# Optimization experiments

Hardware: AMD Instinct MI355X
Metric: run time of the kernel (lower is better)

Reference implementation:

```python
import jax, jax.numpy as jnp
import numpy as np

D = 1024

def setup_inputs() -> dict:
    key = jax.random.key(0)
    ks = jax.random.split(key, 7)
    s = 1.0 / np.sqrt(D)
    x = jax.random.normal(ks[0], (8, 2048, D), dtype=jnp.float32)
    Wq = jax.random.uniform(ks[1], (D, D), jnp.float32, -s, s)
    bq = jax.random.uniform(ks[2], (D,), jnp.float32, -s, s)
    Wk = jax.random.uniform(ks[3], (D, D), jnp.float32, -s, s)
    bk = jax.random.uniform(ks[4], (D,), jnp.float32, -s, s)
    Wv = jax.random.uniform(ks[5], (D, D), jnp.float32, -s, s)
    bv = jax.random.uniform(ks[6], (D,), jnp.float32, -s, s)
    return {"x": x, "Wq": Wq, "bq": bq, "Wk": Wk, "bk": bk, "Wv": Wv, "bv": bv}

def reference(x, Wq, bq, Wk, bk, Wv, bv):
    # x: [B, N, D]; Linear weights stored [D, D] used as x @ W + b (W = torch weight.T)
    q = x @ Wq + bq
    k = x @ Wk + bk
    v = x @ Wv + bv
    scores = jnp.einsum('bnd,bmd->bnm', q, k) / jnp.sqrt(jnp.float32(x.shape[-1]))
    attn = jax.nn.softmax(scores, axis=2)
    return jnp.einsum('bnm,bmd->bnd', attn, v)
```

## Files before the change

kernel.cpp:

```cpp
#include <hip/hip_runtime.h>
#include <hip/hip_bf16.h>

typedef unsigned short u16;
typedef short bf16x8 __attribute__((ext_vector_type(8)));
typedef float f32x16 __attribute__((ext_vector_type(16)));
typedef unsigned short u16x8 __attribute__((ext_vector_type(8)));
typedef unsigned short u16x4 __attribute__((ext_vector_type(4)));

__device__ __forceinline__ u16 f2bf(float f) {
    unsigned u = __float_as_uint(f);
    return (u16)((u + 0x7FFFu + ((u >> 16) & 1u)) >> 16);
}
__device__ __forceinline__ float bf2f(u16 h) {
    return __uint_as_float(((unsigned)h) << 16);
}

__global__ __launch_bounds__(256) void cast_f32_bf16(const float4* __restrict__ src,
                                                     ushort4* __restrict__ dst, int n4) {
    int i = blockIdx.x * 256 + threadIdx.x;
    if (i < n4) {
        float4 v = src[i];
        ushort4 o;
        o.x = f2bf(v.x); o.y = f2bf(v.y); o.z = f2bf(v.z); o.w = f2bf(v.w);
        dst[i] = o;
    }
}

__global__ __launch_bounds__(256) void transpose_cast3(const float* __restrict__ W0,
                                                       const float* __restrict__ W1,
                                                       const float* __restrict__ W2,
                                                       u16* __restrict__ WT) {
    __shared__ float t[32][33];
    const float* W = (blockIdx.z == 0) ? W0 : (blockIdx.z == 1) ? W1 : W2;
    u16* Wt = WT + (long)blockIdx.z * 1048576;
    int bx = blockIdx.x * 32;
    int by = blockIdx.y * 32;
    int tx = threadIdx.x, ty = threadIdx.y;
    for (int r = ty; r < 32; r += 8)
        t[r][tx] = W[(by + r) * 1024 + bx + tx];
    __syncthreads();
    for (int r = ty; r < 32; r += 8)
        Wt[(long)(bx + r) * 1024 + by + tx] = f2bf(t[tx][r]);
}

template <int MODE>
__global__ __launch_bounds__(256)
void gemm_bt(const u16* __restrict__ A, int lda, long sA,
             const u16* __restrict__ Bt, int ldb, long sB,
             const float* __restrict__ bq_, const float* __restrict__ bk_,
             const float* __restrict__ bv_,
             void* __restrict__ Cout, void* __restrict__ Cout2,
             int ldc, long sC, int Kdim, float scale)
{
    __shared__ __align__(16) u16 As[128 * 64];
    __shared__ __align__(16) u16 Bs[128 * 64];
    const int tid  = threadIdx.x;
    const int wave = tid >> 6;
    const int lane = tid & 63;
    const int m32  = lane & 31;
    const int hi   = lane >> 5;

    const int gx = gridDim.x, gy = gridDim.y;
    int flat = (blockIdx.z * gy + blockIdx.y) * gx + blockIdx.x;
    int total = gx * gy * gridDim.z;
    int tile = (flat & 7) * (total >> 3) + (flat >> 3);
    const int bx = tile % gx;
    const int by = (tile / gx) % gy;
    const int bz = tile / (gx * gy);

    const u16* Ab = A + (long)bz * sA;
    const u16* Bb = Bt + (long)bz * sB;
    const int row0 = by * 128;
    const int col0 = bx * 128;
    const int wr = (wave & 1) * 64;
    const int wc = (wave >> 1) * 64;

    f32x16 acc[2][2] = {};

    int arow[2], brow[2], asw[2], bsw[2];
#pragma unroll
    for (int t = 0; t < 2; ++t) {
        arow[t] = wr + t * 32 + m32;
        brow[t] = wc + t * 32 + m32;
        asw[t] = arow[t] & 7;
        bsw[t] = brow[t] & 7;
    }

    for (int k0 = 0; k0 < Kdim; k0 += 64) {
#pragma unroll
        for (int it = 0; it < 4; ++it) {
            int c = it * 256 + tid;
            int r = c >> 3;
            int kc = (c & 7) ^ (r & 7);
            const u16* ga = Ab + (long)(row0 + r) * lda + (k0 + kc * 8);
            __builtin_amdgcn_global_load_lds(
                (const __attribute__((address_space(1))) void*)ga,
                (__attribute__((address_space(3))) void*)(&As[c * 8]), 16, 0, 0);
            const u16* gb = Bb + (long)(col0 + r) * ldb + (k0 + kc * 8);
            __builtin_amdgcn_global_load_lds(
                (const __attribute__((address_space(1))) void*)gb,
                (__attribute__((address_space(3))) void*)(&Bs[c * 8]), 16, 0, 0);
        }
        __syncthreads();
#pragma unroll
        for (int kh = 0; kh < 4; ++kh) {
            bf16x8 af[2], bfr[2];
#pragma unroll
            for (int t = 0; t < 2; ++t) {
                int qa = (kh * 2 + hi) ^ asw[t];
                int qb = (kh * 2 + hi) ^ bsw[t];
                af[t]  = *(const bf16x8*)&As[arow[t] * 64 + qa * 8];
                bfr[t] = *(const bf16x8*)&Bs[brow[t] * 64 + qb * 8];
            }
#pragma unroll
            for (int i = 0; i < 2; ++i)
#pragma unroll
                for (int j = 0; j < 2; ++j)
                    acc[i][j] = __builtin_amdgcn_mfma_f32_32x32x16_bf16(
                        af[i], bfr[j], acc[i][j], 0, 0, 0);
        }
        __syncthreads();
    }

    if (MODE == 0) {
        if (col0 < 2048) {
            const float* bp = (col0 < 1024) ? bq_ : bk_;
#pragma unroll
            for (int i = 0; i < 2; ++i) {
#pragma unroll
                for (int j = 0; j < 2; ++j) {
                    int col = col0 + wc + j * 32 + m32;
                    float badd = bp[col & 1023];
#pragma unroll
                    for (int g = 0; g < 4; ++g) {
                        int rbase = row0 + wr + i * 32 + 4 * hi + 8 * g;
#pragma unroll
                        for (int rr = 0; rr < 4; ++rr)
                            ((u16*)Cout)[(long)(rbase + rr) * 2048 + col] =
                                f2bf(acc[i][j][g * 4 + rr] + badd);
                    }
                }
            }
        } else {
#pragma unroll
            for (int i = 0; i < 2; ++i) {
#pragma unroll
                for (int j = 0; j < 2; ++j) {
                    int d = col0 + wc + j * 32 + m32 - 2048;
                    float badd = bv_[d];
#pragma unroll
                    for (int g = 0; g < 4; ++g) {
                        int rbase = row0 + wr + i * 32 + 4 * hi + 8 * g;
                        int b = rbase >> 11, m = rbase & 2047;
                        u16x4 pk;
#pragma unroll
                        for (int rr = 0; rr < 4; ++rr)
                            pk[rr] = f2bf(acc[i][j][g * 4 + rr] + badd);
                        *(u16x4*)((u16*)Cout2 + ((long)b << 21) + ((long)d << 11) + m) = pk;
                    }
                }
            }
        }
    } else {
#pragma unroll
        for (int i = 0; i < 2; ++i) {
#pragma unroll
            for (int j = 0; j < 2; ++j) {
                int col = col0 + wc + j * 32 + m32;
#pragma unroll
                for (int g = 0; g < 4; ++g) {
                    int rbase = row0 + wr + i * 32 + 4 * hi + 8 * g;
#pragma unroll
                    for (int rr = 0; rr < 4; ++rr) {
                        int row = rbase + rr;
                        float v = acc[i][j][g * 4 + rr];
                        if (MODE == 2) {
                            ((u16*)Cout)[(long)bz * sC + (long)row * ldc + col] = f2bf(v * scale);
                        } else {
                            ((float*)Cout)[(long)bz * sC + (long)row * ldc + col] = v;
                        }
                    }
                }
            }
        }
    }
}

__global__ __launch_bounds__(256) void softmax_rows(u16* __restrict__ S) {
    __shared__ float red[4];
    const long row = blockIdx.x;
    u16* p = S + row * 2048;
    const int tid = threadIdx.x;
    const int lane = tid & 63, wv = tid >> 6;

    u16x8 raw = *(const u16x8*)(p + tid * 8);
    float v[8];
#pragma unroll
    for (int i = 0; i < 8; ++i) v[i] = bf2f(raw[i]);

    float m = -1e30f;
#pragma unroll
    for (int i = 0; i < 8; ++i) m = fmaxf(m, v[i]);
    for (int off = 32; off > 0; off >>= 1) m = fmaxf(m, __shfl_down(m, off));
    if (lane == 0) red[wv] = m;
    __syncthreads();
    m = fmaxf(fmaxf(red[0], red[1]), fmaxf(red[2], red[3]));

    float s = 0.0f;
#pragma unroll
    for (int i = 0; i < 8; ++i) { v[i] = __expf(v[i] - m); s += v[i]; }
    for (int off = 32; off > 0; off >>= 1) s += __shfl_down(s, off);
    __syncthreads();
    if (lane == 0) red[wv] = s;
    __syncthreads();
    s = red[0] + red[1] + red[2] + red[3];
    float inv = 1.0f / s;

    u16x8 o;
#pragma unroll
    for (int i = 0; i < 8; ++i) o[i] = f2bf(v[i] * inv);
    *(u16x8*)(p + tid * 8) = o;
}

extern "C" void kernel_launch(void* const* d_in, const int* in_sizes, int n_in,
                              void* d_out, int out_size, void* d_ws, size_t ws_size,
                              hipStream_t stream) {
    const float* x  = (const float*)d_in[0];
    const float* Wq = (const float*)d_in[1];
    const float* bq = (const float*)d_in[2];
    const float* Wk = (const float*)d_in[3];
    const float* bk = (const float*)d_in[4];
    const float* Wv = (const float*)d_in[5];
    const float* bv = (const float*)d_in[6];
    float* out = (float*)d_out;

    char* ws = (char*)d_ws;
    u16* xb = (u16*)(ws);
    u16* WT = (u16*)(ws + 33554432);
    u16* QK = (u16*)(ws + 39845888);
    u16* Vt = (u16*)(ws + 106954752);
    u16* S  = (u16*)(ws + 140509184);

    cast_f32_bf16<<<16384, 256, 0, stream>>>((const float4*)x, (ushort4*)xb, 4194304);
    dim3 tg(32, 32, 3), tb(32, 8);
    transpose_cast3<<<tg, tb, 0, stream>>>(Wq, Wk, Wv, WT);

    dim3 gp(24, 128, 1);
    gemm_bt<0><<<gp, 256, 0, stream>>>(xb, 1024, 0, WT, 1024, 0,
                                       bq, bk, bv, QK, Vt, 0, 0, 1024, 1.0f);

    dim3 gs(16, 16, 8);
    gemm_bt<2><<<gs, 256, 0, stream>>>(QK, 2048, 2048L * 2048, QK + 1024, 2048, 2048L * 2048,
                                       nullptr, nullptr, nullptr, S, nullptr,
                                       2048, 2048L * 2048, 1024, 0.03125f);

    softmax_rows<<<16384, 256, 0, stream>>>(S);

    dim3 gv(8, 16, 8);
    gemm_bt<3><<<gv, 256, 0, stream>>>(S, 2048, 2048L * 2048, Vt, 2048, 1024L * 2048,
                                       nullptr, nullptr, nullptr, out, nullptr,
                                       1024, 2048L * 1024, 2048, 1.0f);
}
```

Measured before the change: 424.0 us.

## Restructure GEMM to 256x256 tiles with 4-stage async LDS pipeline

Rewrites the shared GEMM kernel used for the QKV projection, QK^T and PV products. It now uses 512-thread blocks computing 256x256 output tiles with BK=32 and 16x16x32 bf16 MFMAs. A 4-deep ring of LDS buffers is filled via global_load_lds with explicit vmcnt waits, so loads overlap compute instead of sync-load-sync per k-step. The aim is more data reuse per block and better latency hiding. In exchange it uses 128KB of LDS and about 128 accumulator VGPRs per thread, which limits occupancy to one block per CU. Each block also covers more of the output, so fewer blocks are launched.

Result: faster. 394.4 us (-7.0%).

```diff
diff --git a/kernel.cpp b/kernel.cpp
--- a/kernel.cpp
+++ b/kernel.cpp
@@ -3,7 +3,7 @@
 
 typedef unsigned short u16;
 typedef short bf16x8 __attribute__((ext_vector_type(8)));
-typedef float f32x16 __attribute__((ext_vector_type(16)));
+typedef float f32x4 __attribute__((ext_vector_type(4)));
 typedef unsigned short u16x8 __attribute__((ext_vector_type(8)));
 typedef unsigned short u16x4 __attribute__((ext_vector_type(4)));
 
@@ -43,8 +43,20 @@
         Wt[(long)(bx + r) * 1024 + by + tx] = f2bf(t[tx][r]);
 }
 
+#define GLL16(g, l)                                                     \
+    __builtin_amdgcn_global_load_lds(                                   \
+        (const __attribute__((address_space(1))) void*)(g),             \
+        (__attribute__((address_space(3))) void*)(l), 16, 0, 0)
+
+#define PIPE_WAIT_BAR(vmstr)                                            \
+    do {                                                                \
+        asm volatile("s_waitcnt " vmstr " lgkmcnt(0)" ::: "memory");    \
+        __builtin_amdgcn_s_barrier();                                   \
+        asm volatile("" ::: "memory");                                  \
+    } while (0)
+
 template <int MODE>
-__global__ __launch_bounds__(256)
+__global__ __launch_bounds__(512, 2)
 void gemm_bt(const u16* __restrict__ A, int lda, long sA,
              const u16* __restrict__ Bt, int ldb, long sB,
              const float* __restrict__ bq_, const float* __restrict__ bk_,
@@ -52,13 +64,13 @@
              void* __restrict__ Cout, void* __restrict__ Cout2,
              int ldc, long sC, int Kdim, float scale)
 {
-    __shared__ __align__(16) u16 As[128 * 64];
-    __shared__ __align__(16) u16 Bs[128 * 64];
+    __shared__ __align__(16) u16 lds[4 * 16384];
+
     const int tid  = threadIdx.x;
     const int wave = tid >> 6;
     const int lane = tid & 63;
-    const int m32  = lane & 31;
-    const int hi   = lane >> 5;
+    const int lrow = lane & 15;
+    const int kc   = lane >> 4;
 
     const int gx = gridDim.x, gy = gridDim.y;
     int flat = (blockIdx.z * gy + blockIdx.y) * gx + blockIdx.x;
@@ -70,116 +82,121 @@
 
     const u16* Ab = A + (long)bz * sA;
     const u16* Bb = Bt + (long)bz * sB;
-    const int row0 = by * 128;
-    const int col0 = bx * 128;
-    const int wr = (wave & 1) * 64;
+    const int row0 = by * 256;
+    const int col0 = bx * 256;
+    const int wr = (wave & 1) * 128;
     const int wc = (wave >> 1) * 64;
 
-    f32x16 acc[2][2] = {};
-
-    int arow[2], brow[2], asw[2], bsw[2];
-#pragma unroll
-    for (int t = 0; t < 2; ++t) {
-        arow[t] = wr + t * 32 + m32;
-        brow[t] = wc + t * 32 + m32;
-        asw[t] = arow[t] & 7;
-        bsw[t] = brow[t] & 7;
-    }
-
-    for (int k0 = 0; k0 < Kdim; k0 += 64) {
-#pragma unroll
-        for (int it = 0; it < 4; ++it) {
-            int c = it * 256 + tid;
-            int r = c >> 3;
-            int kc = (c & 7) ^ (r & 7);
-            const u16* ga = Ab + (long)(row0 + r) * lda + (k0 + kc * 8);
-            __builtin_amdgcn_global_load_lds(
-                (const __attribute__((address_space(1))) void*)ga,
-                (__attribute__((address_space(3))) void*)(&As[c * 8]), 16, 0, 0);
-            const u16* gb = Bb + (long)(col0 + r) * ldb + (k0 + kc * 8);
-            __builtin_amdgcn_global_load_lds(
-                (const __attribute__((address_space(1))) void*)gb,
-                (__attribute__((address_space(3))) void*)(&Bs[c * 8]), 16, 0, 0);
-        }
-        __syncthreads();
-#pragma unroll
-        for (int kh = 0; kh < 4; ++kh) {
-            bf16x8 af[2], bfr[2];
-#pragma unroll
-            for (int t = 0; t < 2; ++t) {
-                int qa = (kh * 2 + hi) ^ asw[t];
-                int qb = (kh * 2 + hi) ^ bsw[t];
-                af[t]  = *(const bf16x8*)&As[arow[t] * 64 + qa * 8];
-                bfr[t] = *(const bf16x8*)&Bs[brow[t] * 64 + qb * 8];
-            }
-#pragma unroll
-            for (int i = 0; i < 2; ++i)
-#pragma unroll
-                for (int j = 0; j < 2; ++j)
-                    acc[i][j] = __builtin_amdgcn_mfma_f32_32x32x16_bf16(
-                        af[i], bfr[j], acc[i][j], 0, 0, 0);
-        }
-        __syncthreads();
-    }
-
+    const int rS = tid >> 2;
+    const int cS = (tid & 3) ^ ((tid >> 3) & 3);
+    const u16* pa0 = Ab + (long)(row0 + rS) * lda + cS * 8;
+    const u16* pa1 = pa0 + (long)128 * lda;
+    const u16* pb0 = Bb + (long)(col0 + rS) * ldb + cS * 8;
+    const u16* pb1 = pb0 + (long)128 * ldb;
+    const int dA0 = tid * 8, dA1 = 4096 + tid * 8;
+    const int dB0 = 8192 + tid * 8, dB1 = 12288 + tid * 8;
+
+    int offA[8], offB[4];
+#pragma unroll
+    for (int mf = 0; mf < 8; ++mf) {
+        int r = wr + mf * 16 + lrow;
+        offA[mf] = r * 32 + (kc ^ ((r >> 1) & 3)) * 8;
+    }
+#pragma unroll
+    for (int nf = 0; nf < 4; ++nf) {
+        int r = wc + nf * 16 + lrow;
+        offB[nf] = 8192 + r * 32 + (kc ^ ((r >> 1) & 3)) * 8;
+    }
+
+    f32x4 acc[8][4] = {};
+
+    auto stage = [&](int t) {
+        u16* lb = &lds[(t & 3) * 16384];
+        int ko = t * 32;
+        GLL16(pa0 + ko, lb + dA0);
+        GLL16(pa1 + ko, lb + dA1);
+        GLL16(pb0 + ko, lb + dB0);
+        GLL16(pb1 + ko, lb + dB1);
+    };
+
+    auto compute = [&](int t) {
+        const u16* lb = &lds[(t & 3) * 16384];
+        bf16x8 af[8], bfr[4];
+#pragma unroll
+        for (int nf = 0; nf < 4; ++nf) bfr[nf] = *(const bf16x8*)&lb[offB[nf]];
+#pragma unroll
+        for (int mf = 0; mf < 8; ++mf) af[mf] = *(const bf16x8*)&lb[offA[mf]];
+        __builtin_amdgcn_s_setprio(1);
+#pragma unroll
+        for (int mf = 0; mf < 8; ++mf)
+#pragma unroll
+            for (int nf = 0; nf < 4; ++nf)
+                acc[mf][nf] = __builtin_amdgcn_mfma_f32_16x16x32_bf16(
+                    af[mf], bfr[nf], acc[mf][nf], 0, 0, 0);
+        __builtin_amdgcn_s_setprio(0);
+    };
+
+    const int NT = Kdim >> 5;
+    stage(0); stage(1); stage(2);
+    for (int t = 0; t < NT - 3; ++t) {
+        PIPE_WAIT_BAR("vmcnt(8)");
+        stage(t + 3);
+        compute(t);
+    }
+    PIPE_WAIT_BAR("vmcnt(8)");
+    compute(NT - 3);
+    PIPE_WAIT_BAR("vmcnt(4)");
+    compute(NT - 2);
+    PIPE_WAIT_BAR("vmcnt(0)");
+    compute(NT - 1);
+
+    const int lq = kc;
     if (MODE == 0) {
         if (col0 < 2048) {
             const float* bp = (col0 < 1024) ? bq_ : bk_;
 #pragma unroll
-            for (int i = 0; i < 2; ++i) {
-#pragma unroll
-                for (int j = 0; j < 2; ++j) {
-                    int col = col0 + wc + j * 32 + m32;
+            for (int mf = 0; mf < 8; ++mf) {
+#pragma unroll
+                for (int nf = 0; nf < 4; ++nf) {
+                    int col = col0 + wc + nf * 16 + lrow;
                     float badd = bp[col & 1023];
-#pragma unroll
-                    for (int g = 0; g < 4; ++g) {
-                        int rbase = row0 + wr + i * 32 + 4 * hi + 8 * g;
-#pragma unroll
-                        for (int rr = 0; rr < 4; ++rr)
-                            ((u16*)Cout)[(long)(rbase + rr) * 2048 + col] =
-                                f2bf(acc[i][j][g * 4 + rr] + badd);
-                    }
+                    int rbase = row0 + wr + mf * 16 + lq * 4;
+#pragma unroll
+                    for (int g = 0; g < 4; ++g)
+                        ((u16*)Cout)[(long)(rbase + g) * 2048 + col] =
+                            f2bf(acc[mf][nf][g] + badd);
                 }
             }
         } else {
 #pragma unroll
-            for (int i = 0; i < 2; ++i) {
-#pragma unroll
-                for (int j = 0; j < 2; ++j) {
-                    int d = col0 + wc + j * 32 + m32 - 2048;
+            for (int mf = 0; mf < 8; ++mf) {
+#pragma unroll
+                for (int nf = 0; nf < 4; ++nf) {
+                    int d = col0 + wc + nf * 16 + lrow - 2048;
                     float badd = bv_[d];
-#pragma unroll
-                    for (int g = 0; g < 4; ++g) {
-                        int rbase = row0 + wr + i * 32 + 4 * hi + 8 * g;
-                        int b = rbase >> 11, m = rbase & 2047;
-                        u16x4 pk;
-#pragma unroll
-                        for (int rr = 0; rr < 4; ++rr)
-                            pk[rr] = f2bf(acc[i][j][g * 4 + rr] + badd);
-                        *(u16x4*)((u16*)Cout2 + ((long)b << 21) + ((long)d << 11) + m) = pk;
-                    }
+                    int rbase = row0 + wr + mf * 16 + lq * 4;
+                    int b = rbase >> 11, m = rbase & 2047;
+                    u16x4 pk;
+#pragma unroll
+                    for (int g = 0; g < 4; ++g) pk[g] = f2bf(acc[mf][nf][g] + badd);
+                    *(u16x4*)((u16*)Cout2 + ((long)b << 21) + ((long)d << 11) + m) = pk;
                 }
             }
         }
     } else {
 #pragma unroll
-        for (int i = 0; i < 2; ++i) {
-#pragma unroll
-            for (int j = 0; j < 2; ++j) {
-                int col = col0 + wc + j * 32 + m32;
+        for (int mf = 0; mf < 8; ++mf) {
+#pragma unroll
+            for (int nf = 0; nf < 4; ++nf) {
+                int col = col0 + wc + nf * 16 + lrow;
+                int rbase = row0 + wr + mf * 16 + lq * 4;
 #pragma unroll
                 for (int g = 0; g < 4; ++g) {
-                    int rbase = row0 + wr + i * 32 + 4 * hi + 8 * g;
-#pragma unroll
-                    for (int rr = 0; rr < 4; ++rr) {
-                        int row = rbase + rr;
-                        float v = acc[i][j][g * 4 + rr];
-                        if (MODE == 2) {
-                            ((u16*)Cout)[(long)bz * sC + (long)row * ldc + col] = f2bf(v * scale);
-                        } else {
-                            ((float*)Cout)[(long)bz * sC + (long)row * ldc + col] = v;
-                        }
-                    }
+                    long idx = (long)bz * sC + (long)(rbase + g) * ldc + col;
+                    if (MODE == 2)
+                        ((u16*)Cout)[idx] = f2bf(acc[mf][nf][g] * scale);
+                    else
+                        ((float*)Cout)[idx] = acc[mf][nf][g];
                 }
             }
         }
@@ -245,19 +262,19 @@
     dim3 tg(32, 32, 3), tb(32, 8);
     transpose_cast3<<<tg, tb, 0, stream>>>(Wq, Wk, Wv, WT);
 
-    dim3 gp(24, 128, 1);
-    gemm_bt<0><<<gp, 256, 0, stream>>>(xb, 1024, 0, WT, 1024, 0,
+    dim3 gp(12, 64, 1);
+    gemm_bt<0><<<gp, 512, 0, stream>>>(xb, 1024, 0, WT, 1024, 0,
                                        bq, bk, bv, QK, Vt, 0, 0, 1024, 1.0f);
 
-    dim3 gs(16, 16, 8);
-    gemm_bt<2><<<gs, 256, 0, stream>>>(QK, 2048, 2048L * 2048, QK + 1024, 2048, 2048L * 2048,
+    dim3 gs(8, 8, 8);
+    gemm_bt<2><<<gs, 512, 0, stream>>>(QK, 2048, 2048L * 2048, QK + 1024, 2048, 2048L * 2048,
                                        nullptr, nullptr, nullptr, S, nullptr,
                                        2048, 2048L * 2048, 1024, 0.03125f);
 
     softmax_rows<<<16384, 256, 0, stream>>>(S);
 
-    dim3 gv(8, 16, 8);
-    gemm_bt<3><<<gv, 256, 0, stream>>>(S, 2048, 2048L * 2048, Vt, 2048, 1024L * 2048,
+    dim3 gv(4, 8, 8);
+    gemm_bt<3><<<gv, 512, 0, stream>>>(S, 2048, 2048L * 2048, Vt, 2048, 1024L * 2048,
                                        nullptr, nullptr, nullptr, out, nullptr,
                                        1024, 2048L * 1024, 2048, 1.0f);
 }
```

## Enlarge GEMM tiles to 256x256 with double-buffered LDS pipeline

Applied to the files above, without the earlier changes.

Switches the bf16 GEMM kernel to 512-thread blocks computing 256x256 tiles, with two LDS buffers. The next K-tile's global-to-LDS loads are issued in quarter-steps, gated by vmcnt waits and barriers, and MFMA priority is raised while computing. The aim is to overlap memory latency with matrix math and raise data reuse per loaded byte. In exchange, each block now uses 128 KB of LDS, and the PV GEMM launches fewer, larger blocks, which reduces parallelism.

Result: slower. 642.0 us (+51.4%).

```diff
diff --git a/kernel.cpp b/kernel.cpp
--- a/kernel.cpp
+++ b/kernel.cpp
@@ -43,8 +43,19 @@
         Wt[(long)(bx + r) * 1024 + by + tx] = f2bf(t[tx][r]);
 }
 
+#define GLL16(g, l)                                                     \
+    __builtin_amdgcn_global_load_lds(                                   \
+        (const __attribute__((address_space(1))) void*)(g),             \
+        (__attribute__((address_space(3))) void*)(l), 16, 0, 0)
+
+#define VMB(n)                                                          \
+    do {                                                                \
+        asm volatile("s_waitcnt vmcnt(" #n ")" ::: "memory");           \
+        __builtin_amdgcn_s_barrier();                                   \
+    } while (0)
+
 template <int MODE>
-__global__ __launch_bounds__(256)
+__global__ __launch_bounds__(512, 2)
 void gemm_bt(const u16* __restrict__ A, int lda, long sA,
              const u16* __restrict__ Bt, int ldb, long sB,
              const float* __restrict__ bq_, const float* __restrict__ bk_,
@@ -52,13 +63,13 @@
              void* __restrict__ Cout, void* __restrict__ Cout2,
              int ldc, long sC, int Kdim, float scale)
 {
-    __shared__ __align__(16) u16 As[128 * 64];
-    __shared__ __align__(16) u16 Bs[128 * 64];
+    __shared__ __align__(16) u16 lds[2 * 32768];
+
     const int tid  = threadIdx.x;
     const int wave = tid >> 6;
     const int lane = tid & 63;
     const int m32  = lane & 31;
-    const int hi   = lane >> 5;
+    const int hi5  = lane >> 5;
 
     const int gx = gridDim.x, gy = gridDim.y;
     int flat = (blockIdx.z * gy + blockIdx.y) * gx + blockIdx.x;
@@ -70,70 +81,77 @@
 
     const u16* Ab = A + (long)bz * sA;
     const u16* Bb = Bt + (long)bz * sB;
-    const int row0 = by * 128;
-    const int col0 = bx * 128;
-    const int wr = (wave & 1) * 64;
+    const int row0 = by * 256;
+    const int col0 = bx * 256;
+    const int wr = (wave & 1) * 128;
     const int wc = (wave >> 1) * 64;
 
-    f32x16 acc[2][2] = {};
-
-    int arow[2], brow[2], asw[2], bsw[2];
-#pragma unroll
-    for (int t = 0; t < 2; ++t) {
-        arow[t] = wr + t * 32 + m32;
-        brow[t] = wc + t * 32 + m32;
-        asw[t] = arow[t] & 7;
-        bsw[t] = brow[t] & 7;
-    }
-
-    for (int k0 = 0; k0 < Kdim; k0 += 64) {
-#pragma unroll
-        for (int it = 0; it < 4; ++it) {
-            int c = it * 256 + tid;
-            int r = c >> 3;
-            int kc = (c & 7) ^ (r & 7);
-            const u16* ga = Ab + (long)(row0 + r) * lda + (k0 + kc * 8);
-            __builtin_amdgcn_global_load_lds(
-                (const __attribute__((address_space(1))) void*)ga,
-                (__attribute__((address_space(3))) void*)(&As[c * 8]), 16, 0, 0);
-            const u16* gb = Bb + (long)(col0 + r) * ldb + (k0 + kc * 8);
-            __builtin_amdgcn_global_load_lds(
-                (const __attribute__((address_space(1))) void*)gb,
-                (__attribute__((address_space(3))) void*)(&Bs[c * 8]), 16, 0, 0);
+    const int r255 = tid & 255;
+    const int hp   = tid >> 8;
+    const u16* paA = Ab + (long)(row0 + r255) * lda + hp * 8;
+    const u16* pbB = Bb + (long)(col0 + r255) * ldb + hp * 8;
+    const int dst8 = tid * 8;
+
+    const int aoff = hi5 * 2048 + (wr + m32) * 8;
+    const int boff = 16384 + hi5 * 2048 + (wc + m32) * 8;
+
+    f32x16 acc[4][2] = {};
+
+#define STAGE_G(t, g)                                                       \
+    do {                                                                    \
+        u16* lb_ = &lds[((t) & 1) * 32768];                                 \
+        const long ko_ = (long)(t) * 64 + (g) * 16;                         \
+        GLL16(paA + ko_, lb_ + (g) * 4096 + dst8);                          \
+        GLL16(pbB + ko_, lb_ + 16384 + (g) * 4096 + dst8);                  \
+    } while (0)
+
+#define READ_MMA(lb_, p)                                                    \
+    do {                                                                    \
+        bf16x8 af[4], bfr[2];                                               \
+        _Pragma("unroll") for (int i = 0; i < 4; ++i)                       \
+            af[i] = *(const bf16x8*)&(lb_)[(p) * 4096 + aoff + i * 256];    \
+        _Pragma("unroll") for (int j = 0; j < 2; ++j)                       \
+            bfr[j] = *(const bf16x8*)&(lb_)[(p) * 4096 + boff + j * 256];   \
+        __builtin_amdgcn_s_setprio(1);                                      \
+        _Pragma("unroll") for (int i = 0; i < 4; ++i)                       \
+        _Pragma("unroll") for (int j = 0; j < 2; ++j)                       \
+            acc[i][j] = __builtin_amdgcn_mfma_f32_32x32x16_bf16(            \
+                af[i], bfr[j], acc[i][j], 0, 0, 0);                         \
+        __builtin_amdgcn_s_setprio(0);                                      \
+    } while (0)
+
+    const int NT = Kdim >> 6;
+    STAGE_G(0, 0); STAGE_G(0, 1); STAGE_G(0, 2); STAGE_G(0, 3);
+
+    for (int t = 0; t < NT - 1; ++t) {
+        const u16* lb = &lds[(t & 1) * 32768];
+#pragma unroll
+        for (int p = 0; p < 4; ++p) {
+            VMB(6);
+            STAGE_G(t + 1, p);
+            READ_MMA(lb, p);
         }
-        __syncthreads();
-#pragma unroll
-        for (int kh = 0; kh < 4; ++kh) {
-            bf16x8 af[2], bfr[2];
-#pragma unroll
-            for (int t = 0; t < 2; ++t) {
-                int qa = (kh * 2 + hi) ^ asw[t];
-                int qb = (kh * 2 + hi) ^ bsw[t];
-                af[t]  = *(const bf16x8*)&As[arow[t] * 64 + qa * 8];
-                bfr[t] = *(const bf16x8*)&Bs[brow[t] * 64 + qb * 8];
-            }
-#pragma unroll
-            for (int i = 0; i < 2; ++i)
-#pragma unroll
-                for (int j = 0; j < 2; ++j)
-                    acc[i][j] = __builtin_amdgcn_mfma_f32_32x32x16_bf16(
-                        af[i], bfr[j], acc[i][j], 0, 0, 0);
-        }
-        __syncthreads();
+    }
+    {
+        const u16* lb = &lds[((NT - 1) & 1) * 32768];
+        VMB(6); READ_MMA(lb, 0);
+        VMB(4); READ_MMA(lb, 1);
+        VMB(2); READ_MMA(lb, 2);
+        VMB(0); READ_MMA(lb, 3);
     }
 
     if (MODE == 0) {
         if (col0 < 2048) {
             const float* bp = (col0 < 1024) ? bq_ : bk_;
 #pragma unroll
-            for (int i = 0; i < 2; ++i) {
+            for (int i = 0; i < 4; ++i) {
 #pragma unroll
                 for (int j = 0; j < 2; ++j) {
                     int col = col0 + wc + j * 32 + m32;
                     float badd = bp[col & 1023];
 #pragma unroll
                     for (int g = 0; g < 4; ++g) {
-                        int rbase = row0 + wr + i * 32 + 4 * hi + 8 * g;
+                        int rbase = row0 + wr + i * 32 + 4 * hi5 + 8 * g;
 #pragma unroll
                         for (int rr = 0; rr < 4; ++rr)
                             ((u16*)Cout)[(long)(rbase + rr) * 2048 + col] =
@@ -143,14 +161,14 @@
             }
         } else {
 #pragma unroll
-            for (int i = 0; i < 2; ++i) {
+            for (int i = 0; i < 4; ++i) {
 #pragma unroll
                 for (int j = 0; j < 2; ++j) {
                     int d = col0 + wc + j * 32 + m32 - 2048;
                     float badd = bv_[d];
 #pragma unroll
                     for (int g = 0; g < 4; ++g) {
-                        int rbase = row0 + wr + i * 32 + 4 * hi + 8 * g;
+                        int rbase = row0 + wr + i * 32 + 4 * hi5 + 8 * g;
                         int b = rbase >> 11, m = rbase & 2047;
                         u16x4 pk;
 #pragma unroll
@@ -163,22 +181,21 @@
         }
     } else {
 #pragma unroll
-        for (int i = 0; i < 2; ++i) {
+        for (int i = 0; i < 4; ++i) {
 #pragma unroll
             for (int j = 0; j < 2; ++j) {
                 int col = col0 + wc + j * 32 + m32;
 #pragma unroll
                 for (int g = 0; g < 4; ++g) {
-                    int rbase = row0 + wr + i * 32 + 4 * hi + 8 * g;
+                    int rbase = row0 + wr + i * 32 + 4 * hi5 + 8 * g;
 #pragma unroll
                     for (int rr = 0; rr < 4; ++rr) {
-                        int row = rbase + rr;
+                        long idx = (long)bz * sC + (long)(rbase + rr) * ldc + col;
                         float v = acc[i][j][g * 4 + rr];
-                        if (MODE == 2) {
-                            ((u16*)Cout)[(long)bz * sC + (long)row * ldc + col] = f2bf(v * scale);
-                        } else {
-                            ((float*)Cout)[(long)bz * sC + (long)row * ldc + col] = v;
-                        }
+                        if (MODE == 2)
+                            ((u16*)Cout)[idx] = f2bf(v * scale);
+                        else
+                            ((float*)Cout)[idx] = v;
                     }
                 }
             }
@@ -245,19 +262,19 @@
     dim3 tg(32, 32, 3), tb(32, 8);
     transpose_cast3<<<tg, tb, 0, stream>>>(Wq, Wk, Wv, WT);
 
-    dim3 gp(24, 128, 1);
-    gemm_bt<0><<<gp, 256, 0, stream>>>(xb, 1024, 0, WT, 1024, 0,
+    dim3 gp(12, 64, 1);
+    gemm_bt<0><<<gp, 512, 0, stream>>>(xb, 1024, 0, WT, 1024, 0,
                                        bq, bk, bv, QK, Vt, 0, 0, 1024, 1.0f);
 
-    dim3 gs(16, 16, 8);
-    gemm_bt<2><<<gs, 256, 0, stream>>>(QK, 2048, 2048L * 2048, QK + 1024, 2048, 2048L * 2048,
+    dim3 gs(8, 8, 8);
+    gemm_bt<2><<<gs, 512, 0, stream>>>(QK, 2048, 2048L * 2048, QK + 1024, 2048, 2048L * 2048,
                                        nullptr, nullptr, nullptr, S, nullptr,
                                        2048, 2048L * 2048, 1024, 0.03125f);
 
     softmax_rows<<<16384, 256, 0, stream>>>(S);
 
-    dim3 gv(8, 16, 8);
-    gemm_bt<3><<<gv, 256, 0, stream>>>(S, 2048, 2048L * 2048, Vt, 2048, 1024L * 2048,
+    dim3 gv(4, 8, 8);
+    gemm_bt<3><<<gv, 512, 0, stream>>>(S, 2048, 2048L * 2048, Vt, 2048, 1024L * 2048,
                                        nullptr, nullptr, nullptr, out, nullptr,
                                        1024, 2048L * 1024, 2048, 1.0f);
 }
```
